# Kernel optimization log

Measured on AMD Instinct MI355X. Metric: run time of the kernel, lower is better.

Reference implementation:

```python
import jax, jax.numpy as jnp
import numpy as np

B, N, M = 16, 4096, 256
Q_DIM, CTX_DIM = 512, 768
HEADS, DIM_HEAD = 8, 64
INNER = HEADS * DIM_HEAD
SCALE = DIM_HEAD ** -0.5


def setup_inputs() -> dict:
    key = jax.random.key(0)
    ks = jax.random.split(key, 8)
    x = jax.random.normal(ks[0], (B, N, Q_DIM), dtype=jnp.float32)
    obj_txt = jax.random.normal(ks[1], (B, M, CTX_DIM), dtype=jnp.float32)
    obj_mask = jax.random.randint(ks[2], (B, N, M), 0, 2) > 0
    obj_vector = jnp.ones((B, M), dtype=bool)  # all-True keeps output finite (see notes)
    Wq = jax.random.normal(ks[3], (Q_DIM, INNER), dtype=jnp.float32) * 0.02
    Wk = jax.random.normal(ks[4], (CTX_DIM, INNER), dtype=jnp.float32) * 0.02
    Wv = jax.random.normal(ks[5], (CTX_DIM, INNER), dtype=jnp.float32) * 0.02
    Wo = jax.random.normal(ks[6], (INNER, Q_DIM), dtype=jnp.float32) * 0.02
    bo = jnp.zeros((Q_DIM,), dtype=jnp.float32)
    return {"x": x, "obj_txt": obj_txt, "obj_mask": obj_mask, "obj_vector": obj_vector,
            "Wq": Wq, "Wk": Wk, "Wv": Wv, "Wo": Wo, "bo": bo}


def reference(x, obj_txt, obj_mask, obj_vector, Wq, Wk, Wv, Wo, bo):
    b, n, _ = x.shape
    m = obj_txt.shape[1]
    q = (x @ Wq).reshape(b, n, HEADS, DIM_HEAD)          # [B,N,H,C]
    k = (obj_txt @ Wk).reshape(b, m, HEADS, DIM_HEAD)    # [B,M,H,C]
    v = (obj_txt @ Wv).reshape(b, m, HEADS, DIM_HEAD)
    sim = jnp.einsum('bnhc,bmhc->bhnm', q, k) * SCALE    # [B,H,N,M]
    neg = -jnp.finfo(sim.dtype).max
    # pre-softmax mask (obj_vector broadcasts over heads and queries)
    sim = jnp.where(obj_vector[:, None, None, :], sim, neg)
    # NOTE: original computes sim.softmax(-1) but then discards it, using the
    # pre-softmax masked sim with ~obj_mask positions set to 0 as the attention.
    attn = jnp.where(obj_mask[:, None, :, :], sim, jnp.array(0.0, sim.dtype))
    out = jnp.einsum('bhnm,bmhc->bnhc', attn, v).reshape(b, n, INNER)
    return out @ Wo + bo
```

## Files before the change

kernel.cpp:

```cpp
#include <hip/hip_runtime.h>

typedef unsigned short u16;
typedef unsigned char u8;
typedef unsigned int u32;
typedef unsigned long long u64;
typedef __attribute__((ext_vector_type(4))) float floatx4;
typedef __attribute__((ext_vector_type(8))) __bf16 bf16x8;

#define GLD_LDS(SRC, DST) __builtin_amdgcn_global_load_lds( \
    (const __attribute__((address_space(1))) void*)(SRC),   \
    (__attribute__((address_space(3))) void*)(DST), 16, 0, 0)

static __device__ __forceinline__ u16 f2bf(float f) {
  return __builtin_bit_cast(u16, (__bf16)f);
}
static __device__ __forceinline__ u32 pk2bf(float a, float b) {
  return (u32)f2bf(a) | ((u32)f2bf(b) << 16);
}
static __device__ __forceinline__ floatx4 mfma16(bf16x8 a, bf16x8 b, floatx4 c) {
  return __builtin_amdgcn_mfma_f32_16x16x32_bf16(a, b, c, 0, 0, 0);
}


__global__ void detect_mask_kernel(const unsigned int* __restrict__ m, int* __restrict__ flag) {
  __shared__ int sh[4];
  int t = threadIdx.x;
  int any = 0;
  for (int i = t; i < 16384; i += 256) any |= ((m[i] & 0xFFFFFF00u) != 0u) ? 1 : 0;
  unsigned long long b = __ballot(any != 0);
  if ((t & 63) == 0) sh[t >> 6] = (b != 0ull) ? 1 : 0;
  __syncthreads();
  if (t == 0) flag[0] = (sh[0] | sh[1] | sh[2] | sh[3]);
}

__global__ __launch_bounds__(256) void convert_x_kernel(const float* __restrict__ x,
                                                        u16* __restrict__ xb) {
  for (int u = blockIdx.x * 256 + threadIdx.x; u < 4194304; u += 524288) {
    const float4* p = reinterpret_cast<const float4*>(x + (size_t)u * 8);
    float4 f0 = p[0], f1 = p[1];
    bf16x8 pk;
    pk[0] = (__bf16)f0.x; pk[1] = (__bf16)f0.y; pk[2] = (__bf16)f0.z; pk[3] = (__bf16)f0.w;
    pk[4] = (__bf16)f1.x; pk[5] = (__bf16)f1.y; pk[6] = (__bf16)f1.z; pk[7] = (__bf16)f1.w;
    *reinterpret_cast<bf16x8*>(xb + (size_t)u * 8) = pk;
  }
}

__global__ __launch_bounds__(256) void prep_weights_kernel(
    const float* __restrict__ Wq, const float* __restrict__ Wk,
    const float* __restrict__ Wv, const float* __restrict__ Wo,
    u16* __restrict__ WqT, u16* __restrict__ WkT,
    u16* __restrict__ WvT, u16* __restrict__ WoT) {
  int z = blockIdx.y;
  const float* src = (z == 0) ? Wq : (z == 1) ? Wk : (z == 2) ? Wv : Wo;
  u16* dst = (z == 0) ? WqT : (z == 1) ? WkT : (z == 2) ? WvT : WoT;
  int K = (z == 1 || z == 2) ? 768 : 512;
  int nk64 = K >> 6;
  int tile = blockIdx.x;
  int kt = tile % nk64, ntile = tile / nk64;
  if (ntile >= 8) return;
  int k0 = kt * 64, n0 = ntile * 64;
  float scale = (z == 0) ? 0.125f : 1.f;
  __shared__ u16 sh[64 * 65];
  int t = threadIdx.x;
#pragma unroll
  for (int i = 0; i < 16; ++i) {
    int kk = i * 4 + (t >> 6), nn = t & 63;
    float v = src[(size_t)(k0 + kk) * 512 + n0 + nn] * scale;
    sh[kk * 65 + nn] = f2bf(v);
  }
  __syncthreads();
#pragma unroll
  for (int i = 0; i < 16; ++i) {
    int nn = i * 4 + (t >> 6), kk = t & 63;
    dst[(size_t)(n0 + nn) * K + k0 + kk] = sh[kk * 65 + nn];
  }
}

__global__ __launch_bounds__(256) void gemm_q_kernel(
    const u16* __restrict__ A, const u16* __restrict__ Bt, u16* __restrict__ Cout) {
  __shared__ u16 As[2][4096];
  __shared__ u16 Bs[2][8192];
  int bid = blockIdx.x;
  int m0 = (bid >> 1) * 128, n0 = (bid & 1) * 256;
  int t = threadIdx.x, lane = t & 63;
  int w = t >> 6, wr = w >> 1, wc = w & 1, lr = lane & 15, lg = lane >> 4;
  floatx4 acc[4][8];
#pragma unroll
  for (int i = 0; i < 4; ++i)
#pragma unroll
    for (int j = 0; j < 8; ++j) acc[i][j] = (floatx4){0.f, 0.f, 0.f, 0.f};

  auto stage = [&](int kt, int bf) {
    int k0 = kt * 32;
#pragma unroll
    for (int i = 0; i < 2; ++i) {
      int idx = (i * 4 + w) * 64 + lane;
      int row = idx >> 2, g = idx & 3;
      int gs = g ^ ((row >> 1) & 3);
      const u16* src = A + (size_t)(m0 + row) * 512 + k0 + gs * 8;
      char* dst = ((char*)&As[0][0]) + bf * 8192 + (i * 4 + w) * 1024;
      GLD_LDS(src, dst);
    }
#pragma unroll
    for (int i = 0; i < 4; ++i) {
      int idx = (i * 4 + w) * 64 + lane;
      int row = idx >> 2, g = idx & 3;
      int gs = g ^ ((row >> 1) & 3);
      const u16* src = Bt + (size_t)(n0 + row) * 512 + k0 + gs * 8;
      char* dst = ((char*)&Bs[0][0]) + bf * 16384 + (i * 4 + w) * 1024;
      GLD_LDS(src, dst);
    }
  };

  stage(0, 0);
  __syncthreads();
  for (int kt = 0; kt < 16; ++kt) {
    int cur = kt & 1;
    if (kt + 1 < 16) stage(kt + 1, cur ^ 1);
    bf16x8 av[4];
#pragma unroll
    for (int i = 0; i < 4; ++i) {
      int r = wr * 64 + i * 16 + lr;
      int ga = lg ^ ((r >> 1) & 3);
      av[i] = *reinterpret_cast<const bf16x8*>(&As[cur][r * 32 + ga * 8]);
    }
#pragma unroll
    for (int j = 0; j < 8; ++j) {
      int rb = wc * 128 + j * 16 + lr;
      int gb = lg ^ ((rb >> 1) & 3);
      bf16x8 bv = *reinterpret_cast<const bf16x8*>(&Bs[cur][rb * 32 + gb * 8]);
#pragma unroll
      for (int i = 0; i < 4; ++i) acc[i][j] = mfma16(bv, av[i], acc[i][j]);
    }
    __syncthreads();
  }
#pragma unroll
  for (int i = 0; i < 4; ++i)
#pragma unroll
    for (int j = 0; j < 8; ++j) {
      int n_row = m0 + wr * 64 + i * 16 + lr;
      int colb = n0 + wc * 128 + j * 16 + lg * 4;
      ushort4 pk4;
      pk4.x = f2bf(acc[i][j][0]); pk4.y = f2bf(acc[i][j][1]);
      pk4.z = f2bf(acc[i][j][2]); pk4.w = f2bf(acc[i][j][3]);
      *reinterpret_cast<ushort4*>(&Cout[(size_t)n_row * 512 + colb]) = pk4;
    }
}

__global__ __launch_bounds__(256) void gemm_kv_kernel(
    const float* __restrict__ A, const u16* __restrict__ Bt0, const u16* __restrict__ Bt1,
    u16* __restrict__ C0, u16* __restrict__ C1) {
  const u16* Bt = Bt0;
  u16* Cout = C0;
  int mode = 0;
  if (blockIdx.z == 1) { Bt = Bt1; Cout = C1; mode = 2; }
  __shared__ float Asf[2][4096];
  __shared__ u16 Bs[2][4096];
  int m0 = blockIdx.x * 128, n0 = blockIdx.y * 128;
  int t = threadIdx.x, lane = t & 63;
  int w = t >> 6, wr = w >> 1, wc = w & 1, lr = lane & 15, lg = lane >> 4;
  floatx4 acc[4][4];
#pragma unroll
  for (int i = 0; i < 4; ++i)
#pragma unroll
    for (int j = 0; j < 4; ++j) acc[i][j] = (floatx4){0.f, 0.f, 0.f, 0.f};

  auto stage = [&](int kt, int bf) {
    int k0 = kt * 32;
#pragma unroll
    for (int i = 0; i < 4; ++i) {
      int idx = (i * 4 + w) * 64 + lane;
      int row = idx >> 3, g = idx & 7;
      int gs = g ^ (row & 7);
      const float* src = A + (size_t)(m0 + row) * 768 + k0 + gs * 4;
      char* dst = ((char*)&Asf[0][0]) + bf * 16384 + (i * 4 + w) * 1024;
      GLD_LDS(src, dst);
    }
#pragma unroll
    for (int i = 0; i < 2; ++i) {
      int idx = (i * 4 + w) * 64 + lane;
      int row = idx >> 2, g = idx & 3;
      int gs = g ^ ((row >> 1) & 3);
      const u16* src = Bt + (size_t)(n0 + row) * 768 + k0 + gs * 8;
      char* dst = ((char*)&Bs[0][0]) + bf * 8192 + (i * 4 + w) * 1024;
      GLD_LDS(src, dst);
    }
  };

  stage(0, 0);
  __syncthreads();
  for (int kt = 0; kt < 24; ++kt) {
    int cur = kt & 1;
    if (kt + 1 < 24) stage(kt + 1, cur ^ 1);
    bf16x8 av[4];
#pragma unroll
    for (int i = 0; i < 4; ++i) {
      int r = wr * 64 + i * 16 + lr;
      int g0 = (2 * lg) ^ (r & 7), g1 = (2 * lg + 1) ^ (r & 7);
      float4 f0 = *reinterpret_cast<const float4*>(&Asf[cur][r * 32 + g0 * 4]);
      float4 f1 = *reinterpret_cast<const float4*>(&Asf[cur][r * 32 + g1 * 4]);
      bf16x8 pk;
      pk[0] = (__bf16)f0.x; pk[1] = (__bf16)f0.y; pk[2] = (__bf16)f0.z; pk[3] = (__bf16)f0.w;
      pk[4] = (__bf16)f1.x; pk[5] = (__bf16)f1.y; pk[6] = (__bf16)f1.z; pk[7] = (__bf16)f1.w;
      av[i] = pk;
    }
#pragma unroll
    for (int j = 0; j < 4; ++j) {
      int rb = wc * 64 + j * 16 + lr;
      int gb = lg ^ ((rb >> 1) & 3);
      bf16x8 bv = *reinterpret_cast<const bf16x8*>(&Bs[cur][rb * 32 + gb * 8]);
#pragma unroll
      for (int i = 0; i < 4; ++i) acc[i][j] = mfma16(bv, av[i], acc[i][j]);
    }
    __syncthreads();
  }
#pragma unroll
  for (int i = 0; i < 4; ++i)
#pragma unroll
    for (int j = 0; j < 4; ++j) {
      int n_row = m0 + wr * 64 + i * 16 + lr;
      int colb = n0 + wc * 64 + j * 16 + lg * 4;
      if (mode == 0) {
        ushort4 pk4;
        pk4.x = f2bf(acc[i][j][0]); pk4.y = f2bf(acc[i][j][1]);
        pk4.z = f2bf(acc[i][j][2]); pk4.w = f2bf(acc[i][j][3]);
        *reinterpret_cast<ushort4*>(&Cout[(size_t)n_row * 512 + colb]) = pk4;
      } else {
        int bb = n_row >> 8, mm = n_row & 255;
#pragma unroll
        for (int r = 0; r < 4; ++r) {
          int col = colb + r;
          int hh = col >> 6, cc = col & 63;
          Cout[(((size_t)(bb * 8 + hh)) * 64 + cc) * 256 + mm] = f2bf(acc[i][j][r]);
        }
      }
    }
}

__global__ __launch_bounds__(256) void gemm_o_kernel(
    const u16* __restrict__ A, const u16* __restrict__ Bt, const float* __restrict__ bo,
    float* __restrict__ out) {
  __shared__ u16 As[2][4096];
  __shared__ u16 Bs[2][8192];
  int bid = blockIdx.x;
  int m0 = (bid >> 1) * 128, n0 = (bid & 1) * 256;
  int t = threadIdx.x, lane = t & 63;
  int w = t >> 6, wr = w >> 1, wc = w & 1, lr = lane & 15, lg = lane >> 4;
  floatx4 acc[4][8];
#pragma unroll
  for (int i = 0; i < 4; ++i)
#pragma unroll
    for (int j = 0; j < 8; ++j) acc[i][j] = (floatx4){0.f, 0.f, 0.f, 0.f};

  auto stage = [&](int kt, int bf) {
    int k0 = kt * 32;
#pragma unroll
    for (int i = 0; i < 2; ++i) {
      int idx = (i * 4 + w) * 64 + lane;
      int row = idx >> 2, g = idx & 3;
      int gs = g ^ ((row >> 1) & 3);
      const u16* src = A + (size_t)(m0 + row) * 512 + k0 + gs * 8;
      char* dst = ((char*)&As[0][0]) + bf * 8192 + (i * 4 + w) * 1024;
      GLD_LDS(src, dst);
    }
#pragma unroll
    for (int i = 0; i < 4; ++i) {
      int idx = (i * 4 + w) * 64 + lane;
      int row = idx >> 2, g = idx & 3;
      int gs = g ^ ((row >> 1) & 3);
      const u16* src = Bt + (size_t)(n0 + row) * 512 + k0 + gs * 8;
      char* dst = ((char*)&Bs[0][0]) + bf * 16384 + (i * 4 + w) * 1024;
      GLD_LDS(src, dst);
    }
  };

  stage(0, 0);
  __syncthreads();
  for (int kt = 0; kt < 16; ++kt) {
    int cur = kt & 1;
    if (kt + 1 < 16) stage(kt + 1, cur ^ 1);
    bf16x8 av[4];
#pragma unroll
    for (int i = 0; i < 4; ++i) {
      int r = wr * 64 + i * 16 + lr;
      int ga = lg ^ ((r >> 1) & 3);
      av[i] = *reinterpret_cast<const bf16x8*>(&As[cur][r * 32 + ga * 8]);
    }
#pragma unroll
    for (int j = 0; j < 8; ++j) {
      int rb = wc * 128 + j * 16 + lr;
      int gb = lg ^ ((rb >> 1) & 3);
      bf16x8 bv = *reinterpret_cast<const bf16x8*>(&Bs[cur][rb * 32 + gb * 8]);
#pragma unroll
      for (int i = 0; i < 4; ++i) acc[i][j] = mfma16(bv, av[i], acc[i][j]);
    }
    __syncthreads();
  }
#pragma unroll
  for (int i = 0; i < 4; ++i)
#pragma unroll
    for (int j = 0; j < 8; ++j) {
      int n_row = m0 + wr * 64 + i * 16 + lr;
      int colb = n0 + wc * 128 + j * 16 + lg * 4;
      float4 bv4 = *reinterpret_cast<const float4*>(&bo[colb]);
      float4 st;
      st.x = acc[i][j][0] + bv4.x; st.y = acc[i][j][1] + bv4.y;
      st.z = acc[i][j][2] + bv4.z; st.w = acc[i][j][3] + bv4.w;
      *reinterpret_cast<float4*>(&out[(size_t)n_row * 512 + colb]) = st;
    }
}

__global__ __launch_bounds__(512, 2) void attn_kernel(
    u16* qoin, const u16* __restrict__ Kb, const u16* __restrict__ Vt,
    const void* __restrict__ maskp, const int* __restrict__ flag) {
  __shared__ u16 k_lds[16384];
  __shared__ u16 v_lds[16384];
  __shared__ u16 ubuf[8][1024];
  int id = blockIdx.y * 32 + blockIdx.x;
  int xcd = id & 7, j0 = id >> 3;
  int bIdx = 2 * xcd + (j0 >> 5);
  int nx = j0 & 31;
  int lane = threadIdx.x & 63, w = threadIdx.x >> 6, lr = lane & 15, lg = lane >> 4;
  int n0w = nx * 128 + w * 16;
  bool mByte = flag[0] != 0;

  u64 mb;
  {
    int n = n0w + lr;
    size_t base = ((size_t)(bIdx * 4096 + n)) * 256;
    u64 bits = 0;
    if (mByte) {
      const u8* mp = (const u8*)maskp + base;
      for (int mt = 0; mt < 16; ++mt) {
        u32 dw = *(const u32*)(mp + mt * 16 + lg * 4);
#pragma unroll
        for (int r = 0; r < 4; ++r)
          if ((dw >> (8 * r)) & 0xFFu) bits |= (1ull << (mt * 4 + r));
      }
    } else {
      const int* mp = (const int*)maskp + base;
      for (int mt = 0; mt < 16; ++mt) {
        int4 q = *(const int4*)(mp + mt * 16 + lg * 4);
        if (q.x) bits |= 1ull << (mt * 4 + 0);
        if (q.y) bits |= 1ull << (mt * 4 + 1);
        if (q.z) bits |= 1ull << (mt * 4 + 2);
        if (q.w) bits |= 1ull << (mt * 4 + 3);
      }
    }
    mb = bits;
  }

  for (int h = 0; h < 8; ++h) {
    __syncthreads();
#pragma unroll
    for (int i = 0; i < 4; ++i) {
      int idx = (i * 8 + w) * 64 + lane;
      int m = idx >> 3, g = idx & 7;
      int gs = g ^ (m & 7);
      const u16* src = Kb + ((size_t)(bIdx * 256 + m)) * 512 + h * 64 + gs * 8;
      char* dst = ((char*)k_lds) + (i * 8 + w) * 1024;
      GLD_LDS(src, dst);
    }
#pragma unroll
    for (int i = 0; i < 4; ++i) {
      int idx = (i * 8 + w) * 64 + lane;
      int c = idx >> 5, g = idx & 31;
      int gs = (g & 24) | ((g & 7) ^ (c & 7));
      const u16* src = Vt + (((size_t)(bIdx * 8 + h)) * 64 + c) * 256 + gs * 8;
      char* dst = ((char*)v_lds) + (i * 8 + w) * 1024;
      GLD_LDS(src, dst);
    }
    bf16x8 qf[2];
#pragma unroll
    for (int ks = 0; ks < 2; ++ks)
      qf[ks] = *reinterpret_cast<const bf16x8*>(
          qoin + ((size_t)(bIdx * 4096 + n0w + lr)) * 512 + h * 64 + ks * 32 + lg * 8);
    __syncthreads();

    floatx4 acc2[4];
#pragma unroll
    for (int ct = 0; ct < 4; ++ct) acc2[ct] = (floatx4){0.f, 0.f, 0.f, 0.f};

    for (int ch = 0; ch < 8; ++ch) {
      floatx4 s[2];
#pragma unroll
      for (int mt2 = 0; mt2 < 2; ++mt2) s[mt2] = (floatx4){0.f, 0.f, 0.f, 0.f};
#pragma unroll
      for (int mt2 = 0; mt2 < 2; ++mt2) {
        int m = (ch * 2 + mt2) * 16 + lr;
#pragma unroll
        for (int ks = 0; ks < 2; ++ks) {
          int g = ks * 4 + lg;
          bf16x8 af = *reinterpret_cast<const bf16x8*>(&k_lds[m * 64 + ((g ^ (m & 7)) << 3)]);
          s[mt2] = mfma16(af, qf[ks], s[mt2]);
        }
      }
      u32* pb = (u32*)&ubuf[w][0];
#pragma unroll
      for (int mt2 = 0; mt2 < 2; ++mt2) {
        int sh = (ch * 2 + mt2) * 4;
        float v0 = ((mb >> (sh + 0)) & 1ull) ? s[mt2][0] : 0.f;
        float v1 = ((mb >> (sh + 1)) & 1ull) ? s[mt2][1] : 0.f;
        float v2 = ((mb >> (sh + 2)) & 1ull) ? s[mt2][2] : 0.f;
        float v3 = ((mb >> (sh + 3)) & 1ull) ? s[mt2][3] : 0.f;
        int gm = mt2 * 4 + lg;
        int gmp = gm ^ ((lr & 3) << 1);
        u64 pkd = (u64)pk2bf(v0, v1) | ((u64)pk2bf(v2, v3) << 32);
        *(u64*)(pb + lr * 16 + gmp * 2) = pkd;
      }
      int gmp = (2 * lg) ^ ((lr & 3) << 1);
      bf16x8 pf = *reinterpret_cast<const bf16x8*>(&ubuf[w][lr * 32 + gmp * 4]);
#pragma unroll
      for (int ct = 0; ct < 4; ++ct) {
        int c = ct * 16 + lr;
        int gv = ch * 4 + lg;
        int gvp = (gv & 24) | ((gv & 7) ^ (c & 7));
        bf16x8 vf = *reinterpret_cast<const bf16x8*>(&v_lds[c * 256 + gvp * 8]);
        acc2[ct] = mfma16(pf, vf, acc2[ct]);
      }
    }

#pragma unroll
    for (int ct = 0; ct < 4; ++ct)
#pragma unroll
      for (int r = 0; r < 4; ++r) {
        int c = ct * 16 + lr;
        int n = lg * 4 + r;
        int cg = c >> 3;
        ubuf[w][n * 64 + ((cg ^ (n & 7)) << 3) + (c & 7)] = f2bf(acc2[ct][r]);
      }
#pragma unroll
    for (int half = 0; half < 2; ++half) {
      int np = (lane >> 3) + half * 8;
      int cc = lane & 7;
      bf16x8 frag = *reinterpret_cast<const bf16x8*>(&ubuf[w][np * 64 + ((cc ^ (np & 7)) << 3)]);
      *reinterpret_cast<bf16x8*>(
          qoin + ((size_t)(bIdx * 4096 + n0w + np)) * 512 + h * 64 + cc * 8) = frag;
    }
  }
}

extern "C" void kernel_launch(void* const* d_in, const int* in_sizes, int n_in,
                              void* d_out, int out_size, void* d_ws, size_t ws_size,
                              hipStream_t stream) {
  const float* x = (const float*)d_in[0];
  const float* obj_txt = (const float*)d_in[1];
  const void* obj_mask = d_in[2];
  const float* Wq = (const float*)d_in[4];
  const float* Wk = (const float*)d_in[5];
  const float* Wv = (const float*)d_in[6];
  const float* Wo = (const float*)d_in[7];
  const float* bo = (const float*)d_in[8];
  float* out = (float*)d_out;

  char* ws = (char*)d_ws;
  u16* Qb = (u16*)ws;
  u16* Kb = (u16*)(ws + 67108864);
  u16* Vt = (u16*)(ws + 71303168);
  u16* WqT = (u16*)(ws + 75497472);
  u16* WkT = (u16*)(ws + 76021760);
  u16* WvT = (u16*)(ws + 76808192);
  u16* WoT = (u16*)(ws + 77594624);
  int* flag = (int*)(ws + 78118912);
  u16* xb = (u16*)d_out;

  detect_mask_kernel<<<1, 256, 0, stream>>>((const unsigned int*)obj_mask, flag);
  prep_weights_kernel<<<dim3(96, 4, 1), 256, 0, stream>>>(Wq, Wk, Wv, Wo, WqT, WkT, WvT, WoT);
  convert_x_kernel<<<2048, 256, 0, stream>>>(x, xb);
  gemm_q_kernel<<<1024, 256, 0, stream>>>(xb, WqT, Qb);
  gemm_kv_kernel<<<dim3(32, 4, 2), 256, 0, stream>>>(obj_txt, WkT, WvT, Kb, Vt);
  attn_kernel<<<dim3(32, 16, 1), 512, 0, stream>>>(Qb, Kb, Vt, obj_mask, flag);
  gemm_o_kernel<<<1024, 256, 0, stream>>>(Qb, WoT, bo, out);
}
```

Baseline: 301.6 us.

## Give each attention wave two query tiles and split heads across blocks

Each wave in the attention kernel now processes 32 query rows as two 16-row tiles instead of 16 rows. Each K fragment and V fragment read from LDS therefore feeds two MFMAs. To keep the same block count, the grid gains a z dimension and each block handles only four of the eight heads, so staging K/V into LDS is amortised over twice as many rows. In exchange, the per-row mask bits are loaded and packed in both head-half blocks, so mask global traffic doubles, and register pressure rises from the doubled accumulators and Q fragments.

```diff
diff --git a/kernel.cpp b/kernel.cpp
--- a/kernel.cpp
+++ b/kernel.cpp
@@ -316,17 +316,19 @@
   __shared__ u16 k_lds[16384];
   __shared__ u16 v_lds[16384];
   __shared__ u16 ubuf[8][1024];
-  int id = blockIdx.y * 32 + blockIdx.x;
+  int id = blockIdx.z * 256 + blockIdx.y * 16 + blockIdx.x;
   int xcd = id & 7, j0 = id >> 3;
   int bIdx = 2 * xcd + (j0 >> 5);
-  int nx = j0 & 31;
+  int nx = (j0 & 31) >> 1;
+  int hh = j0 & 1;
   int lane = threadIdx.x & 63, w = threadIdx.x >> 6, lr = lane & 15, lg = lane >> 4;
-  int n0w = nx * 128 + w * 16;
+  int n0w = nx * 256 + w * 32;
   bool mByte = flag[0] != 0;
 
-  u64 mb;
-  {
-    int n = n0w + lr;
+  u64 mb[2];
+#pragma unroll
+  for (int nt = 0; nt < 2; ++nt) {
+    int n = n0w + nt * 16 + lr;
     size_t base = ((size_t)(bIdx * 4096 + n)) * 256;
     u64 bits = 0;
     if (mByte) {
@@ -347,10 +349,11 @@
         if (q.w) bits |= 1ull << (mt * 4 + 3);
       }
     }
-    mb = bits;
-  }
-
-  for (int h = 0; h < 8; ++h) {
+    mb[nt] = bits;
+  }
+
+  for (int hi = 0; hi < 4; ++hi) {
+    int h = hh * 4 + hi;
     __syncthreads();
 #pragma unroll
     for (int i = 0; i < 4; ++i) {
@@ -370,21 +373,27 @@
       char* dst = ((char*)v_lds) + (i * 8 + w) * 1024;
       GLD_LDS(src, dst);
     }
-    bf16x8 qf[2];
-#pragma unroll
-    for (int ks = 0; ks < 2; ++ks)
-      qf[ks] = *reinterpret_cast<const bf16x8*>(
-          qoin + ((size_t)(bIdx * 4096 + n0w + lr)) * 512 + h * 64 + ks * 32 + lg * 8);
+    bf16x8 qf[2][2];
+#pragma unroll
+    for (int nt = 0; nt < 2; ++nt)
+#pragma unroll
+      for (int ks = 0; ks < 2; ++ks)
+        qf[nt][ks] = *reinterpret_cast<const bf16x8*>(
+            qoin + ((size_t)(bIdx * 4096 + n0w + nt * 16 + lr)) * 512 + h * 64 + ks * 32 + lg * 8);
     __syncthreads();
 
-    floatx4 acc2[4];
-#pragma unroll
-    for (int ct = 0; ct < 4; ++ct) acc2[ct] = (floatx4){0.f, 0.f, 0.f, 0.f};
+    floatx4 acc2[2][4];
+#pragma unroll
+    for (int nt = 0; nt < 2; ++nt)
+#pragma unroll
+      for (int ct = 0; ct < 4; ++ct) acc2[nt][ct] = (floatx4){0.f, 0.f, 0.f, 0.f};
 
     for (int ch = 0; ch < 8; ++ch) {
-      floatx4 s[2];
-#pragma unroll
-      for (int mt2 = 0; mt2 < 2; ++mt2) s[mt2] = (floatx4){0.f, 0.f, 0.f, 0.f};
+      floatx4 s[2][2];
+#pragma unroll
+      for (int nt = 0; nt < 2; ++nt)
+#pragma unroll
+        for (int mt2 = 0; mt2 < 2; ++mt2) s[nt][mt2] = (floatx4){0.f, 0.f, 0.f, 0.f};
 #pragma unroll
       for (int mt2 = 0; mt2 < 2; ++mt2) {
         int m = (ch * 2 + mt2) * 16 + lr;
@@ -392,50 +401,61 @@
         for (int ks = 0; ks < 2; ++ks) {
           int g = ks * 4 + lg;
           bf16x8 af = *reinterpret_cast<const bf16x8*>(&k_lds[m * 64 + ((g ^ (m & 7)) << 3)]);
-          s[mt2] = mfma16(af, qf[ks], s[mt2]);
+#pragma unroll
+          for (int nt = 0; nt < 2; ++nt) s[nt][mt2] = mfma16(af, qf[nt][ks], s[nt][mt2]);
         }
       }
       u32* pb = (u32*)&ubuf[w][0];
 #pragma unroll
-      for (int mt2 = 0; mt2 < 2; ++mt2) {
-        int sh = (ch * 2 + mt2) * 4;
-        float v0 = ((mb >> (sh + 0)) & 1ull) ? s[mt2][0] : 0.f;
-        float v1 = ((mb >> (sh + 1)) & 1ull) ? s[mt2][1] : 0.f;
-        float v2 = ((mb >> (sh + 2)) & 1ull) ? s[mt2][2] : 0.f;
-        float v3 = ((mb >> (sh + 3)) & 1ull) ? s[mt2][3] : 0.f;
-        int gm = mt2 * 4 + lg;
-        int gmp = gm ^ ((lr & 3) << 1);
-        u64 pkd = (u64)pk2bf(v0, v1) | ((u64)pk2bf(v2, v3) << 32);
-        *(u64*)(pb + lr * 16 + gmp * 2) = pkd;
-      }
-      int gmp = (2 * lg) ^ ((lr & 3) << 1);
-      bf16x8 pf = *reinterpret_cast<const bf16x8*>(&ubuf[w][lr * 32 + gmp * 4]);
+      for (int nt = 0; nt < 2; ++nt)
+#pragma unroll
+        for (int mt2 = 0; mt2 < 2; ++mt2) {
+          int sh = (ch * 2 + mt2) * 4;
+          float v0 = ((mb[nt] >> (sh + 0)) & 1ull) ? s[nt][mt2][0] : 0.f;
+          float v1 = ((mb[nt] >> (sh + 1)) & 1ull) ? s[nt][mt2][1] : 0.f;
+          float v2 = ((mb[nt] >> (sh + 2)) & 1ull) ? s[nt][mt2][2] : 0.f;
+          float v3 = ((mb[nt] >> (sh + 3)) & 1ull) ? s[nt][mt2][3] : 0.f;
+          int gm = mt2 * 4 + lg;
+          int gmp = gm ^ (lane & 6);
+          u64 pkd = (u64)pk2bf(v0, v1) | ((u64)pk2bf(v2, v3) << 32);
+          *(u64*)(pb + nt * 256 + lr * 16 + gmp * 2) = pkd;
+        }
+      bf16x8 pf[2];
+#pragma unroll
+      for (int nt = 0; nt < 2; ++nt) {
+        int g0 = (2 * lg) ^ (lane & 6);
+        pf[nt] = *reinterpret_cast<const bf16x8*>(&ubuf[w][nt * 512 + lr * 32 + g0 * 4]);
+      }
 #pragma unroll
       for (int ct = 0; ct < 4; ++ct) {
         int c = ct * 16 + lr;
         int gv = ch * 4 + lg;
         int gvp = (gv & 24) | ((gv & 7) ^ (c & 7));
         bf16x8 vf = *reinterpret_cast<const bf16x8*>(&v_lds[c * 256 + gvp * 8]);
-        acc2[ct] = mfma16(pf, vf, acc2[ct]);
-      }
-    }
-
-#pragma unroll
-    for (int ct = 0; ct < 4; ++ct)
-#pragma unroll
-      for (int r = 0; r < 4; ++r) {
-        int c = ct * 16 + lr;
-        int n = lg * 4 + r;
-        int cg = c >> 3;
-        ubuf[w][n * 64 + ((cg ^ (n & 7)) << 3) + (c & 7)] = f2bf(acc2[ct][r]);
-      }
-#pragma unroll
-    for (int half = 0; half < 2; ++half) {
-      int np = (lane >> 3) + half * 8;
-      int cc = lane & 7;
-      bf16x8 frag = *reinterpret_cast<const bf16x8*>(&ubuf[w][np * 64 + ((cc ^ (np & 7)) << 3)]);
-      *reinterpret_cast<bf16x8*>(
-          qoin + ((size_t)(bIdx * 4096 + n0w + np)) * 512 + h * 64 + cc * 8) = frag;
+#pragma unroll
+        for (int nt = 0; nt < 2; ++nt) acc2[nt][ct] = mfma16(pf[nt], vf, acc2[nt][ct]);
+      }
+    }
+
+#pragma unroll
+    for (int nt = 0; nt < 2; ++nt) {
+#pragma unroll
+      for (int ct = 0; ct < 4; ++ct)
+#pragma unroll
+        for (int r = 0; r < 4; ++r) {
+          int c = ct * 16 + lr;
+          int n = lg * 4 + r;
+          int cg = c >> 3;
+          ubuf[w][n * 64 + ((cg ^ (n & 7)) << 3) + (c & 7)] = f2bf(acc2[nt][ct][r]);
+        }
+#pragma unroll
+      for (int half = 0; half < 2; ++half) {
+        int np = (lane >> 3) + half * 8;
+        int cc = lane & 7;
+        bf16x8 frag = *reinterpret_cast<const bf16x8*>(&ubuf[w][np * 64 + ((cc ^ (np & 7)) << 3)]);
+        *reinterpret_cast<bf16x8*>(
+            qoin + ((size_t)(bIdx * 4096 + n0w + nt * 16 + np)) * 512 + h * 64 + cc * 8) = frag;
+      }
     }
   }
 }
@@ -469,6 +489,6 @@
   convert_x_kernel<<<2048, 256, 0, stream>>>(x, xb);
   gemm_q_kernel<<<1024, 256, 0, stream>>>(xb, WqT, Qb);
   gemm_kv_kernel<<<dim3(32, 4, 2), 256, 0, stream>>>(obj_txt, WkT, WvT, Kb, Vt);
-  attn_kernel<<<dim3(32, 16, 1), 512, 0, stream>>>(Qb, Kb, Vt, obj_mask, flag);
+  attn_kernel<<<dim3(16, 16, 2), 512, 0, stream>>>(Qb, Kb, Vt, obj_mask, flag);
   gemm_o_kernel<<<1024, 256, 0, stream>>>(Qb, WoT, bo, out);
 }
```

Result: slower. 311.7 us (+3.3%).

## Rewrite attention with 32x32 MFMA, register P via permlane, premasked words

Applied to the files above, without the earlier changes.

The attention kernel switches from 16x16x32 to 32x32x16 bf16 MFMA with 4 waves of 32 rows each. The masked score tile is repacked into the PV operand in registers with permlane32_swap instead of a round trip through LDS. V is read straight from global memory rather than staged in LDS. A new pre-pass expands the boolean mask into 16-bit AND masks stored in spare space in the output buffer, so masking becomes a bitwise AND after a packed bf16 convert. The costs are an extra kernel that writes a 32MB mask buffer and uncached global V loads inside the inner loop.

```diff
diff --git a/kernel.cpp b/kernel.cpp
--- a/kernel.cpp
+++ b/kernel.cpp
@@ -5,7 +5,10 @@
 typedef unsigned int u32;
 typedef unsigned long long u64;
 typedef __attribute__((ext_vector_type(4))) float floatx4;
+typedef __attribute__((ext_vector_type(16))) float floatx16;
 typedef __attribute__((ext_vector_type(8))) __bf16 bf16x8;
+typedef __attribute__((ext_vector_type(2))) unsigned int u32x2;
+typedef __attribute__((ext_vector_type(4))) unsigned int u32x4;
 
 #define GLD_LDS(SRC, DST) __builtin_amdgcn_global_load_lds( \
     (const __attribute__((address_space(1))) void*)(SRC),   \
@@ -14,11 +17,16 @@
 static __device__ __forceinline__ u16 f2bf(float f) {
   return __builtin_bit_cast(u16, (__bf16)f);
 }
-static __device__ __forceinline__ u32 pk2bf(float a, float b) {
-  return (u32)f2bf(a) | ((u32)f2bf(b) << 16);
-}
 static __device__ __forceinline__ floatx4 mfma16(bf16x8 a, bf16x8 b, floatx4 c) {
   return __builtin_amdgcn_mfma_f32_16x16x32_bf16(a, b, c, 0, 0, 0);
+}
+static __device__ __forceinline__ floatx16 mfma32(bf16x8 a, bf16x8 b, floatx16 c) {
+  return __builtin_amdgcn_mfma_f32_32x32x16_bf16(a, b, c, 0, 0, 0);
+}
+static __device__ __forceinline__ u32 cvtpk(float lo, float hi) {
+  u32 r;
+  asm("v_cvt_pk_bf16_f32 %0, %1, %2" : "=v"(r) : "v"(lo), "v"(hi));
+  return r;
 }
 
 
@@ -31,6 +39,33 @@
   if ((t & 63) == 0) sh[t >> 6] = (b != 0ull) ? 1 : 0;
   __syncthreads();
   if (t == 0) flag[0] = (sh[0] | sh[1] | sh[2] | sh[3]);
+}
+
+__global__ __launch_bounds__(256) void prep_maskw_kernel(
+    const void* __restrict__ maskp, const int* __restrict__ flag, u32* __restrict__ maskw) {
+  int gid = blockIdx.x * 256 + threadIdx.x;
+  int row = gid >> 5, idx = gid & 31;
+  int mt = idx >> 2, sub = (idx >> 1) & 1, hi = idx & 1;
+  int mbase = mt * 32 + sub * 16 + hi * 4;
+  u32x4 wq;
+  if (flag[0] != 0) {
+    const u8* mp = (const u8*)maskp + (size_t)row * 256 + mbase;
+    u32 c0 = *(const u32*)mp;
+    u32 c1 = *(const u32*)(mp + 8);
+    wq[0] = ((c0 & 0xFFu) ? 0xFFFFu : 0u) | ((c0 & 0xFF00u) ? 0xFFFF0000u : 0u);
+    wq[1] = ((c0 & 0xFF0000u) ? 0xFFFFu : 0u) | ((c0 & 0xFF000000u) ? 0xFFFF0000u : 0u);
+    wq[2] = ((c1 & 0xFFu) ? 0xFFFFu : 0u) | ((c1 & 0xFF00u) ? 0xFFFF0000u : 0u);
+    wq[3] = ((c1 & 0xFF0000u) ? 0xFFFFu : 0u) | ((c1 & 0xFF000000u) ? 0xFFFF0000u : 0u);
+  } else {
+    const int* mp = (const int*)maskp + (size_t)row * 256 + mbase;
+    int4 A = *(const int4*)mp;
+    int4 Bv = *(const int4*)(mp + 8);
+    wq[0] = (A.x ? 0xFFFFu : 0u) | (A.y ? 0xFFFF0000u : 0u);
+    wq[1] = (A.z ? 0xFFFFu : 0u) | (A.w ? 0xFFFF0000u : 0u);
+    wq[2] = (Bv.x ? 0xFFFFu : 0u) | (Bv.y ? 0xFFFF0000u : 0u);
+    wq[3] = (Bv.z ? 0xFFFFu : 0u) | (Bv.w ? 0xFFFF0000u : 0u);
+  }
+  *reinterpret_cast<u32x4*>(maskw + (size_t)row * 128 + idx * 4) = wq;
 }
 
 __global__ __launch_bounds__(256) void convert_x_kernel(const float* __restrict__ x,
@@ -310,132 +345,89 @@
     }
 }
 
-__global__ __launch_bounds__(512, 2) void attn_kernel(
+__global__ __launch_bounds__(256) void attn_kernel(
     u16* qoin, const u16* __restrict__ Kb, const u16* __restrict__ Vt,
-    const void* __restrict__ maskp, const int* __restrict__ flag) {
+    const u32* __restrict__ maskw) {
   __shared__ u16 k_lds[16384];
-  __shared__ u16 v_lds[16384];
-  __shared__ u16 ubuf[8][1024];
+  __shared__ u16 ubuf[4][2304];
   int id = blockIdx.y * 32 + blockIdx.x;
   int xcd = id & 7, j0 = id >> 3;
   int bIdx = 2 * xcd + (j0 >> 5);
   int nx = j0 & 31;
-  int lane = threadIdx.x & 63, w = threadIdx.x >> 6, lr = lane & 15, lg = lane >> 4;
-  int n0w = nx * 128 + w * 16;
-  bool mByte = flag[0] != 0;
-
-  u64 mb;
-  {
-    int n = n0w + lr;
-    size_t base = ((size_t)(bIdx * 4096 + n)) * 256;
-    u64 bits = 0;
-    if (mByte) {
-      const u8* mp = (const u8*)maskp + base;
-      for (int mt = 0; mt < 16; ++mt) {
-        u32 dw = *(const u32*)(mp + mt * 16 + lg * 4);
-#pragma unroll
-        for (int r = 0; r < 4; ++r)
-          if ((dw >> (8 * r)) & 0xFFu) bits |= (1ull << (mt * 4 + r));
-      }
-    } else {
-      const int* mp = (const int*)maskp + base;
-      for (int mt = 0; mt < 16; ++mt) {
-        int4 q = *(const int4*)(mp + mt * 16 + lg * 4);
-        if (q.x) bits |= 1ull << (mt * 4 + 0);
-        if (q.y) bits |= 1ull << (mt * 4 + 1);
-        if (q.z) bits |= 1ull << (mt * 4 + 2);
-        if (q.w) bits |= 1ull << (mt * 4 + 3);
-      }
-    }
-    mb = bits;
-  }
+  int t = threadIdx.x, lane = t & 63, w = t >> 6;
+  int l31 = lane & 31, hi = lane >> 5;
+  int n0w = nx * 128 + w * 32;
+  int nrow = n0w + l31;
+  const u32* mwrow = maskw + (size_t)(bIdx * 4096 + nrow) * 128 + hi * 4;
+  const u16* qrow = qoin + (size_t)(bIdx * 4096 + nrow) * 512 + hi * 8;
+  const u16* vhbase0 = Vt + ((size_t)(bIdx * 8)) * 16384 + (size_t)l31 * 256 + hi * 8;
 
   for (int h = 0; h < 8; ++h) {
     __syncthreads();
 #pragma unroll
-    for (int i = 0; i < 4; ++i) {
-      int idx = (i * 8 + w) * 64 + lane;
-      int m = idx >> 3, g = idx & 7;
+    for (int i = 0; i < 8; ++i) {
+      int u = i * 256 + t;
+      int m = u >> 3, g = u & 7;
       int gs = g ^ (m & 7);
       const u16* src = Kb + ((size_t)(bIdx * 256 + m)) * 512 + h * 64 + gs * 8;
-      char* dst = ((char*)k_lds) + (i * 8 + w) * 1024;
-      GLD_LDS(src, dst);
-    }
-#pragma unroll
-    for (int i = 0; i < 4; ++i) {
-      int idx = (i * 8 + w) * 64 + lane;
-      int c = idx >> 5, g = idx & 31;
-      int gs = (g & 24) | ((g & 7) ^ (c & 7));
-      const u16* src = Vt + (((size_t)(bIdx * 8 + h)) * 64 + c) * 256 + gs * 8;
-      char* dst = ((char*)v_lds) + (i * 8 + w) * 1024;
-      GLD_LDS(src, dst);
-    }
-    bf16x8 qf[2];
-#pragma unroll
-    for (int ks = 0; ks < 2; ++ks)
-      qf[ks] = *reinterpret_cast<const bf16x8*>(
-          qoin + ((size_t)(bIdx * 4096 + n0w + lr)) * 512 + h * 64 + ks * 32 + lg * 8);
+      GLD_LDS(src, ((char*)k_lds) + (i * 4 + w) * 1024);
+    }
+    bf16x8 qf0 = *reinterpret_cast<const bf16x8*>(qrow + h * 64);
+    bf16x8 qf1 = *reinterpret_cast<const bf16x8*>(qrow + h * 64 + 16);
+    bf16x8 qf2 = *reinterpret_cast<const bf16x8*>(qrow + h * 64 + 32);
+    bf16x8 qf3 = *reinterpret_cast<const bf16x8*>(qrow + h * 64 + 48);
     __syncthreads();
 
-    floatx4 acc2[4];
-#pragma unroll
-    for (int ct = 0; ct < 4; ++ct) acc2[ct] = (floatx4){0.f, 0.f, 0.f, 0.f};
-
-    for (int ch = 0; ch < 8; ++ch) {
-      floatx4 s[2];
-#pragma unroll
-      for (int mt2 = 0; mt2 < 2; ++mt2) s[mt2] = (floatx4){0.f, 0.f, 0.f, 0.f};
-#pragma unroll
-      for (int mt2 = 0; mt2 < 2; ++mt2) {
-        int m = (ch * 2 + mt2) * 16 + lr;
-#pragma unroll
-        for (int ks = 0; ks < 2; ++ks) {
-          int g = ks * 4 + lg;
-          bf16x8 af = *reinterpret_cast<const bf16x8*>(&k_lds[m * 64 + ((g ^ (m & 7)) << 3)]);
-          s[mt2] = mfma16(af, qf[ks], s[mt2]);
-        }
+    floatx16 oin0 = (floatx16){0.f};
+    floatx16 oin1 = (floatx16){0.f};
+    const u16* vh = vhbase0 + (size_t)h * 16384;
+
+#pragma unroll
+    for (int mt = 0; mt < 8; ++mt) {
+      int m = mt * 32 + l31;
+      floatx16 s = (floatx16){0.f};
+#pragma unroll
+      for (int ks = 0; ks < 4; ++ks) {
+        int g = ks * 2 + hi;
+        bf16x8 af = *reinterpret_cast<const bf16x8*>(&k_lds[m * 64 + ((g ^ (m & 7)) << 3)]);
+        if (ks == 0) s = mfma32(af, qf0, s);
+        else if (ks == 1) s = mfma32(af, qf1, s);
+        else if (ks == 2) s = mfma32(af, qf2, s);
+        else s = mfma32(af, qf3, s);
       }
-      u32* pb = (u32*)&ubuf[w][0];
-#pragma unroll
-      for (int mt2 = 0; mt2 < 2; ++mt2) {
-        int sh = (ch * 2 + mt2) * 4;
-        float v0 = ((mb >> (sh + 0)) & 1ull) ? s[mt2][0] : 0.f;
-        float v1 = ((mb >> (sh + 1)) & 1ull) ? s[mt2][1] : 0.f;
-        float v2 = ((mb >> (sh + 2)) & 1ull) ? s[mt2][2] : 0.f;
-        float v3 = ((mb >> (sh + 3)) & 1ull) ? s[mt2][3] : 0.f;
-        int gm = mt2 * 4 + lg;
-        int gmp = gm ^ ((lr & 3) << 1);
-        u64 pkd = (u64)pk2bf(v0, v1) | ((u64)pk2bf(v2, v3) << 32);
-        *(u64*)(pb + lr * 16 + gmp * 2) = pkd;
+#pragma unroll
+      for (int sub = 0; sub < 2; ++sub) {
+        u32x4 mw = *reinterpret_cast<const u32x4*>(mwrow + mt * 16 + sub * 8);
+        u32 a0 = cvtpk(s[sub * 8 + 0], s[sub * 8 + 1]) & mw[0];
+        u32 a1 = cvtpk(s[sub * 8 + 2], s[sub * 8 + 3]) & mw[1];
+        u32 b0 = cvtpk(s[sub * 8 + 4], s[sub * 8 + 5]) & mw[2];
+        u32 b1 = cvtpk(s[sub * 8 + 6], s[sub * 8 + 7]) & mw[3];
+        u32x2 r0 = __builtin_amdgcn_permlane32_swap(a0, b0, false, false);
+        u32x2 r1 = __builtin_amdgcn_permlane32_swap(a1, b1, false, false);
+        u32x4 paw;
+        paw[0] = r0[0]; paw[1] = r1[0]; paw[2] = r0[1]; paw[3] = r1[1];
+        bf16x8 pa = __builtin_bit_cast(bf16x8, paw);
+        int moff = mt * 32 + sub * 16;
+        bf16x8 vf0 = *reinterpret_cast<const bf16x8*>(vh + moff);
+        bf16x8 vf1 = *reinterpret_cast<const bf16x8*>(vh + 32 * 256 + moff);
+        oin0 = mfma32(pa, vf0, oin0);
+        oin1 = mfma32(pa, vf1, oin1);
       }
-      int gmp = (2 * lg) ^ ((lr & 3) << 1);
-      bf16x8 pf = *reinterpret_cast<const bf16x8*>(&ubuf[w][lr * 32 + gmp * 4]);
-#pragma unroll
-      for (int ct = 0; ct < 4; ++ct) {
-        int c = ct * 16 + lr;
-        int gv = ch * 4 + lg;
-        int gvp = (gv & 24) | ((gv & 7) ^ (c & 7));
-        bf16x8 vf = *reinterpret_cast<const bf16x8*>(&v_lds[c * 256 + gvp * 8]);
-        acc2[ct] = mfma16(pf, vf, acc2[ct]);
-      }
-    }
-
-#pragma unroll
-    for (int ct = 0; ct < 4; ++ct)
-#pragma unroll
-      for (int r = 0; r < 4; ++r) {
-        int c = ct * 16 + lr;
-        int n = lg * 4 + r;
-        int cg = c >> 3;
-        ubuf[w][n * 64 + ((cg ^ (n & 7)) << 3) + (c & 7)] = f2bf(acc2[ct][r]);
-      }
-#pragma unroll
-    for (int half = 0; half < 2; ++half) {
-      int np = (lane >> 3) + half * 8;
-      int cc = lane & 7;
-      bf16x8 frag = *reinterpret_cast<const bf16x8*>(&ubuf[w][np * 64 + ((cc ^ (np & 7)) << 3)]);
+    }
+
+#pragma unroll
+    for (int r = 0; r < 16; ++r) {
+      int n_off = (r & 3) + 8 * (r >> 2) + 4 * hi;
+      ubuf[w][n_off * 72 + l31] = f2bf(oin0[r]);
+      ubuf[w][n_off * 72 + 32 + l31] = f2bf(oin1[r]);
+    }
+#pragma unroll
+    for (int pass = 0; pass < 4; ++pass) {
+      int prow = lane >> 1;
+      int grp = (lane & 1) * 4 + pass;
+      bf16x8 frag = *reinterpret_cast<const bf16x8*>(&ubuf[w][prow * 72 + grp * 8]);
       *reinterpret_cast<bf16x8*>(
-          qoin + ((size_t)(bIdx * 4096 + n0w + np)) * 512 + h * 64 + cc * 8) = frag;
+          qoin + ((size_t)(bIdx * 4096 + n0w + prow)) * 512 + h * 64 + grp * 8) = frag;
     }
   }
 }
@@ -463,12 +455,14 @@
   u16* WoT = (u16*)(ws + 77594624);
   int* flag = (int*)(ws + 78118912);
   u16* xb = (u16*)d_out;
+  u32* maskw = (u32*)((char*)d_out + 100663296);
 
   detect_mask_kernel<<<1, 256, 0, stream>>>((const unsigned int*)obj_mask, flag);
+  prep_maskw_kernel<<<8192, 256, 0, stream>>>(obj_mask, flag, maskw);
   prep_weights_kernel<<<dim3(96, 4, 1), 256, 0, stream>>>(Wq, Wk, Wv, Wo, WqT, WkT, WvT, WoT);
   convert_x_kernel<<<2048, 256, 0, stream>>>(x, xb);
   gemm_q_kernel<<<1024, 256, 0, stream>>>(xb, WqT, Qb);
   gemm_kv_kernel<<<dim3(32, 4, 2), 256, 0, stream>>>(obj_txt, WkT, WvT, Kb, Vt);
-  attn_kernel<<<dim3(32, 16, 1), 512, 0, stream>>>(Qb, Kb, Vt, obj_mask, flag);
+  attn_kernel<<<dim3(32, 16, 1), 256, 0, stream>>>(Qb, Kb, Vt, maskw);
   gemm_o_kernel<<<1024, 256, 0, stream>>>(Qb, WoT, bo, out);
 }
```

After: 368.7 us. 1.22x slower.
